# Kernel optimization log

Measured on AMD Instinct MI355X. Metric: run time of the kernel, lower is better.

Reference implementation:

```python
import jax, jax.numpy as jnp
import numpy as np

B, L, D = 2, 2048, 1024
H, K = 16, 16
HD = D // H


def setup_inputs() -> dict:
    key = jax.random.key(0)
    k1, k2, k3, k4, k5 = jax.random.split(key, 5)
    x = jax.random.normal(k1, (B, L, D), dtype=jnp.float32)
    # Linear weight (out_features, in_features), small init to keep logits sane
    w_in = jax.random.normal(k2, (3 * D, D), dtype=jnp.float32) * 0.02
    # TISA radial-basis kernel parameters, per (head, kernel)
    kernel_offsets = jax.random.normal(k3, (H, K), dtype=jnp.float32) * 20.0
    kernel_amplitudes = 0.1 + 0.01 * jax.random.normal(k4, (H, K), dtype=jnp.float32)
    kernel_sharpness = 0.1 + 0.01 * jax.random.normal(k5, (H, K), dtype=jnp.float32)
    return {"x": x, "w_in": w_in, "kernel_offsets": kernel_offsets,
            "kernel_amplitudes": kernel_amplitudes, "kernel_sharpness": kernel_sharpness}


def tisa_bias(offsets, amplitudes, sharpness, seq_len):
    # relative positions -(L-1) .. (L-1)  -> per-head RBF positional scores
    rel = jnp.arange(-(seq_len - 1), seq_len, dtype=jnp.float32)  # (2L-1,)
    # scores[h, m] = sum_k amp[h,k] * exp(-|sharp[h,k]| * (off[h,k] - rel[m])^2)
    diff = offsets[:, :, None] - rel[None, None, :]               # (H, K, 2L-1)
    scores = jnp.sum(amplitudes[:, :, None] * jnp.exp(-jnp.abs(sharpness)[:, :, None] * diff * diff), axis=1)  # (H, 2L-1)
    # Toeplitz expansion: bias[h, i, j] = scores[h, (i - j) + (L-1)]
    i = jnp.arange(seq_len)
    idx = i[:, None] - i[None, :] + (seq_len - 1)                 # (L, L)
    return scores[:, idx]                                         # (H, L, L)


def reference(x, w_in, kernel_offsets, kernel_amplitudes, kernel_sharpness):
    b, l, d = x.shape
    proj = jnp.einsum('bld,ed->ble', x, w_in)                     # (B, L, 3D)
    # split: memory = first 2D (k then v), query = last D
    k_, v_, q_ = proj[..., :d], proj[..., d:2 * d], proj[..., 2 * d:]

    def heads(t):
        return t.reshape(b, l, H, HD).transpose(0, 2, 1, 3)       # (B, H, L, HD)

    q, k, v = heads(q_), heads(k_), heads(v_)
    bias = tisa_bias(kernel_offsets, kernel_amplitudes, kernel_sharpness, l)  # (H, L, L)
    scale = 1.0 / np.sqrt(HD).astype(np.float32)
    logits = jnp.einsum('bhld,bhmd->bhlm', q, k) * scale + bias[None]
    attn = jax.nn.softmax(logits, axis=-1)
    out = jnp.einsum('bhlm,bhmd->bhld', attn, v)                  # (B, H, L, HD)
    return out.transpose(0, 2, 1, 3).reshape(b, l, d)             # (B, L, D)
```

## Files before the change

kernel.cpp:

```cpp
#include <hip/hip_runtime.h>
#include <hip/hip_bf16.h>
#include <stdint.h>
#include <stddef.h>


#define NB     2
#define NH     16
#define SL     2048
#define DH     64
#define DMODEL 1024
#define SCP    4096

typedef __attribute__((ext_vector_type(8)))  short bf16x8;
typedef __attribute__((ext_vector_type(4)))  short bf16x4;
typedef __attribute__((ext_vector_type(4)))  float f32x4;
typedef __attribute__((ext_vector_type(16))) float f32x16;

static __device__ __forceinline__ short f2bf(float x) {
  __hip_bfloat16 h = __float2bfloat16(x);
  return *reinterpret_cast<short*>(&h);
}
static __device__ __forceinline__ short f2bf_fast(float x) {
  union { float f; uint32_t u; } v; v.f = x;
  return (short)((v.u + 0x8000u) >> 16);
}
static __device__ __forceinline__ long long bf4_to_ll(bf16x4 v) {
  long long r; __builtin_memcpy(&r, &v, 8); return r;
}
static __device__ __forceinline__ bf16x4 ll_to_bf4(long long v) {
  bf16x4 r; __builtin_memcpy(&r, &v, 8); return r;
}
#define GLD(g, l) __builtin_amdgcn_global_load_lds( \
    (const __attribute__((address_space(1))) void*)(g), \
    (__attribute__((address_space(3))) void*)(l), 16, 0, 0)

__global__ __launch_bounds__(256) void prep_k(
    const float* __restrict__ x, const float* __restrict__ w,
    const float* __restrict__ koff, const float* __restrict__ kamp,
    const float* __restrict__ kshp,
    short* __restrict__ xbf, short* __restrict__ wbf,
    float* __restrict__ scores) {
  const int bx = blockIdx.x, tid = threadIdx.x;
  if (bx < 7168) {
    const float* src = (bx < 4096) ? x : w;
    short* dst       = (bx < 4096) ? xbf : wbf;
    const int i      = (bx < 4096 ? bx : bx - 4096) * 256 + tid;
    float4 a = *(const float4*)(src + (size_t)i * 4);
    bf16x4 o;
    o.x = f2bf(a.x); o.y = f2bf(a.y); o.z = f2bf(a.z); o.w = f2bf(a.w);
    *(bf16x4*)(dst + (size_t)i * 4) = o;
  } else {
    const int idx = bx - 7168;
    const int h = idx >> 4;
    const int r = (idx & 15) * 256 + tid;
    if (r >= 4095) return;
    float rel = (float)(r - (SL - 1));
    float acc = 0.f;
#pragma unroll
    for (int k = 0; k < 16; ++k) {
      float o = koff[h * 16 + k];
      float a = kamp[h * 16 + k];
      float s = fabsf(kshp[h * 16 + k]);
      float d = o - rel;
      acc += a * __expf(-s * d * d);
    }
    scores[h * SCP + r] = acc;
  }
}

__global__ __launch_bounds__(256) void qkv_gemm_k(
    const short* __restrict__ A, const short* __restrict__ Bw,
    __hip_bfloat16* __restrict__ kbuf, __hip_bfloat16* __restrict__ vbufT,
    __hip_bfloat16* __restrict__ qbuf) {
  __shared__ __align__(16) short SM[12288];
  short* As = SM;
  short* Bs = SM + 8192;
  const int tid  = threadIdx.x;
  const int lane = tid & 63;
  const int wv   = tid >> 6;
  const int l15  = lane & 15, quad = lane >> 4;
  const int wm = (wv & 1) * 64, wn = (wv >> 1) * 32;
  const int xt = blockIdx.x, yt = blockIdx.y;
  const int m0 = yt * 128, n0 = xt * 64;
  const int which = xt >> 4;
  const int hh    = xt & 15;

  f32x4 acc[4][2];
#pragma unroll
  for (int r = 0; r < 4; ++r)
#pragma unroll
    for (int c = 0; c < 2; ++c) acc[r][c] = (f32x4){0.f, 0.f, 0.f, 0.f};

  for (int kt = 0; kt < 16; ++kt) {
    const int k0 = kt * 64;
#pragma unroll
    for (int it = 0; it < 4; ++it) {
      const int e8  = it * 256 + tid;
      GLD(A + (size_t)(m0 + (e8 >> 3)) * DMODEL + k0 + (e8 & 7) * 8, &As[e8 * 8]);
    }
#pragma unroll
    for (int it = 0; it < 2; ++it) {
      const int e8  = it * 256 + tid;
      GLD(Bw + (size_t)(n0 + (e8 >> 3)) * DMODEL + k0 + (e8 & 7) * 8, &Bs[e8 * 8]);
    }
    __syncthreads();
#pragma unroll
    for (int ki = 0; ki < 64; ki += 32) {
      bf16x8 af[4], bfv[2];
#pragma unroll
      for (int r = 0; r < 4; ++r)
        af[r] = *(const bf16x8*)&As[(wm + r * 16 + l15) * 64 + ki + quad * 8];
#pragma unroll
      for (int c = 0; c < 2; ++c)
        bfv[c] = *(const bf16x8*)&Bs[(wn + c * 16 + l15) * 64 + ki + quad * 8];
#pragma unroll
      for (int r = 0; r < 4; ++r)
#pragma unroll
        for (int c = 0; c < 2; ++c)
          acc[r][c] = __builtin_amdgcn_mfma_f32_16x16x32_bf16(af[r], bfv[c], acc[r][c], 0, 0, 0);
    }
    __syncthreads();
  }

  const int bb  = m0 >> 11;
  const int llb = m0 & 2047;
  if (which != 1) {
    const float qs = (which == 2) ? 0.125f : 1.0f;
#pragma unroll
    for (int r = 0; r < 4; ++r)
#pragma unroll
      for (int c = 0; c < 2; ++c)
#pragma unroll
        for (int gg = 0; gg < 4; ++gg)
          SM[(wm + r * 16 + quad * 4 + gg) * 72 + wn + c * 16 + l15] =
              f2bf_fast(acc[r][c][gg] * qs);
    __syncthreads();
    __hip_bfloat16* dst = (which == 0) ? kbuf : qbuf;
#pragma unroll
    for (int i = 0; i < 4; ++i) {
      const int cidx = i * 256 + tid;
      const int m = cidx >> 3, ch = cidx & 7;
      bf16x8 val = *(const bf16x8*)&SM[m * 72 + ch * 8];
      *(bf16x8*)&dst[(((size_t)bb * NH + hh) * SL + llb + m) * DH + ch * 8] = val;
    }
  } else {
#pragma unroll
    for (int r = 0; r < 4; ++r)
#pragma unroll
      for (int c = 0; c < 2; ++c) {
        bf16x4 pk;
#pragma unroll
        for (int gg = 0; gg < 4; ++gg) pk[gg] = f2bf_fast(acc[r][c][gg]);
        *(bf16x4*)&SM[(wn + c * 16 + l15) * 136 + wm + r * 16 + quad * 4] = pk;
      }
    __syncthreads();
#pragma unroll
    for (int i = 0; i < 4; ++i) {
      const int cidx = i * 256 + tid;
      const int n = cidx >> 4, ch = cidx & 15;
      bf16x8 val = *(const bf16x8*)&SM[n * 136 + ch * 8];
      *(bf16x8*)&vbufT[(((size_t)bb * NH + hh) * DH + n) * SL + llb + ch * 8] = val;
    }
  }
}

__global__ __launch_bounds__(128, 2) void attn_k(
    const __hip_bfloat16* __restrict__ qbuf, const __hip_bfloat16* __restrict__ kbuf,
    const __hip_bfloat16* __restrict__ vbufT, const float* __restrict__ scores,
    float* __restrict__ out) {
  __shared__ __align__(16) short Ks[64 * 72];
  __shared__ __align__(16) short Vs[64 * 72];
  __shared__ __align__(16) float Bss[2112];
  const int bh   = blockIdx.x;
  const int b    = bh >> 4, h = bh & 15;
  const int tid  = threadIdx.x;
  const int lane = tid & 63;
  const int wv   = tid >> 6;
  const int n32  = lane & 31, hf = lane >> 5;
  const int i0b  = blockIdx.y * 64;
  const int i0   = i0b + wv * 32;
  const __hip_bfloat16* qb = qbuf + (size_t)bh * SL * DH;
  const short* kb = (const short*)(kbuf + (size_t)bh * SL * DH);
  const short* vb = (const short*)(vbufT + (size_t)bh * DH * SL);
  const float* sc = scores + h * SCP;

  {
    const float* bsrc = sc + i0b;
#pragma unroll
    for (int i = 0; i < 4; ++i)
      GLD(bsrc + (size_t)(i * 128 + tid) * 4, &Bss[(i * 128 + tid) * 4]);
    if (tid < 16) GLD(bsrc + (size_t)(512 + tid) * 4, &Bss[(512 + tid) * 4]);
  }

  bf16x8 qf[4];
#pragma unroll
  for (int kc = 0; kc < 4; ++kc)
    qf[kc] = *(const bf16x8*)&qb[(size_t)(i0 + n32) * DH + kc * 16 + hf * 8];

  f32x16 ot[2];
#pragma unroll
  for (int dt = 0; dt < 2; ++dt)
#pragma unroll
    for (int r = 0; r < 16; ++r) ot[dt][r] = 0.f;
  float lsum = 0.f;

  for (int j0 = 0; j0 < SL; j0 += 64) {
    {
      const short* ksrc = kb + (size_t)j0 * DH;
#pragma unroll
      for (int i = 0; i < 4; ++i) {
        int c = i * 128 + tid; int r = c / 9, s = c - r * 9;
        GLD(ksrc + (size_t)r * DH + s * 8, &Ks[c * 8]);
      }
      if (tid < 64) {
        int c = 512 + tid; int r = c / 9, s = c - r * 9;
        GLD(ksrc + (size_t)r * DH + s * 8, &Ks[c * 8]);
      }
    }
    {
#pragma unroll
      for (int i = 0; i < 4; ++i) {
        int c = i * 128 + tid; int r = c / 9, s = c - r * 9;
        GLD(vb + (size_t)r * SL + j0 + s * 8, &Vs[c * 8]);
      }
      if (tid < 64) {
        int c = 512 + tid; int r = c / 9, s = c - r * 9;
        GLD(vb + (size_t)r * SL + j0 + s * 8, &Vs[c * 8]);
      }
    }
    __syncthreads();

#pragma unroll
    for (int kt = 0; kt < 2; ++kt) {
      f32x16 st;
#pragma unroll
      for (int r = 0; r < 16; ++r) st[r] = 0.f;
#pragma unroll
      for (int kc = 0; kc < 4; ++kc) {
        bf16x8 kf = *(const bf16x8*)&Ks[(kt * 32 + n32) * 72 + kc * 16 + hf * 8];
        st = __builtin_amdgcn_mfma_f32_32x32x16_bf16(kf, qf[kc], st, 0, 0, 0);
      }
      bf16x4 pk[4];
      const int tb0 = wv * 32 + n32 - j0 - kt * 32 - 4 * hf + 2047;
#pragma unroll
      for (int g = 0; g < 4; ++g) {
        const int tb = tb0 - 8 * g;
#pragma unroll
        for (int i = 0; i < 4; ++i) {
          const float p = __expf(st[g * 4 + i] + Bss[tb - i]);
          lsum += p;
          pk[g][i] = f2bf_fast(p);
        }
      }
      long long s0 = hf ? bf4_to_ll(pk[0]) : bf4_to_ll(pk[1]);
      bf16x4 r0 = ll_to_bf4(__shfl_xor(s0, 32));
      bf16x8 pf0 = hf == 0 ? __builtin_shufflevector(pk[0], r0, 0, 1, 2, 3, 4, 5, 6, 7)
                           : __builtin_shufflevector(r0, pk[1], 0, 1, 2, 3, 4, 5, 6, 7);
      long long s1 = hf ? bf4_to_ll(pk[2]) : bf4_to_ll(pk[3]);
      bf16x4 r1 = ll_to_bf4(__shfl_xor(s1, 32));
      bf16x8 pf1 = hf == 0 ? __builtin_shufflevector(pk[2], r1, 0, 1, 2, 3, 4, 5, 6, 7)
                           : __builtin_shufflevector(r1, pk[3], 0, 1, 2, 3, 4, 5, 6, 7);
#pragma unroll
      for (int dt = 0; dt < 2; ++dt) {
        const short* vr = &Vs[(dt * 32 + n32) * 72 + kt * 32];
        bf16x8 vf0 = *(const bf16x8*)&vr[hf * 8];
        bf16x8 vf1 = *(const bf16x8*)&vr[16 + hf * 8];
        ot[dt] = __builtin_amdgcn_mfma_f32_32x32x16_bf16(vf0, pf0, ot[dt], 0, 0, 0);
        ot[dt] = __builtin_amdgcn_mfma_f32_32x32x16_bf16(vf1, pf1, ot[dt], 0, 0, 0);
      }
    }
    __syncthreads();
  }

  lsum += __shfl_xor(lsum, 32);
  const float inv = 1.f / lsum;
  float* orow = out + (((size_t)b * SL + i0 + n32) * NH + h) * DH;
#pragma unroll
  for (int dt = 0; dt < 2; ++dt)
#pragma unroll
    for (int g = 0; g < 4; ++g) {
      f32x4 v;
#pragma unroll
      for (int i = 0; i < 4; ++i) v[i] = ot[dt][g * 4 + i] * inv;
      *(f32x4*)&orow[dt * 32 + 8 * g + 4 * hf] = v;
    }
}

extern "C" void kernel_launch(void* const* d_in, const int* in_sizes, int n_in,
                              void* d_out, int out_size, void* d_ws, size_t ws_size,
                              hipStream_t stream) {
  const float* x    = (const float*)d_in[0];
  const float* w    = (const float*)d_in[1];
  const float* koff = (const float*)d_in[2];
  const float* kamp = (const float*)d_in[3];
  const float* kshp = (const float*)d_in[4];
  float* out = (float*)d_out;

  const size_t per = (size_t)NB * NH * SL * DH;
  const size_t nx  = (size_t)NB * SL * DMODEL;
  const size_t nw  = (size_t)3 * DMODEL * DMODEL;

  __hip_bfloat16* kbuf  = (__hip_bfloat16*)d_ws;
  __hip_bfloat16* vbufT = kbuf + per;
  __hip_bfloat16* qbuf  = vbufT + per;
  float* scores = (float*)(qbuf + per);
  short* xbf    = (short*)(scores + (size_t)NH * SCP);
  short* wbf    = xbf + nx;

  prep_k<<<7424, 256, 0, stream>>>(x, w, koff, kamp, kshp, xbf, wbf, scores);
  qkv_gemm_k<<<dim3(48, 32), 256, 0, stream>>>(xbf, wbf, kbuf, vbufT, qbuf);
  attn_k<<<dim3(NB * NH, SL / 64), 128, 0, stream>>>(qbuf, kbuf, vbufT, scores, out);
}
```

Before: 195.1 us.

## Double-buffer K/V tiles in attention and fold log2e into scores for exp2

The attention loop now double-buffers K, V and a small per-tile bias window in LDS, issuing the next tile's async global-to-LDS loads before computing the current tile. This hides load latency and keeps one barrier per iteration. Log2(e) is folded into the Q scale and the TISA scores so softmax can use the native exp2 instruction. s_setprio is raised around the MFMA sections. LDS use roughly doubles for K/V, which may affect occupancy, while the full bias slab is replaced by a 128-float window per tile.

```diff
diff --git a/kernel.cpp b/kernel.cpp
--- a/kernel.cpp
+++ b/kernel.cpp
@@ -10,6 +10,7 @@
 #define DH     64
 #define DMODEL 1024
 #define SCP    4096
+#define LOG2E  1.44269504088896340736f
 
 typedef __attribute__((ext_vector_type(8)))  short bf16x8;
 typedef __attribute__((ext_vector_type(4)))  short bf16x4;
@@ -29,6 +30,13 @@
 }
 static __device__ __forceinline__ bf16x4 ll_to_bf4(long long v) {
   bf16x4 r; __builtin_memcpy(&r, &v, 8); return r;
+}
+static __device__ __forceinline__ float fexp2(float x) {
+#if __has_builtin(__builtin_amdgcn_exp2f)
+  return __builtin_amdgcn_exp2f(x);
+#else
+  return __expf(x * 0.69314718056f);
+#endif
 }
 #define GLD(g, l) __builtin_amdgcn_global_load_lds( \
     (const __attribute__((address_space(1))) void*)(g), \
@@ -64,7 +72,7 @@
       float d = o - rel;
       acc += a * __expf(-s * d * d);
     }
-    scores[h * SCP + r] = acc;
+    scores[h * SCP + r] = acc * LOG2E;
   }
 }
 
@@ -125,7 +133,7 @@
   const int bb  = m0 >> 11;
   const int llb = m0 & 2047;
   if (which != 1) {
-    const float qs = (which == 2) ? 0.125f : 1.0f;
+    const float qs = (which == 2) ? 0.125f * LOG2E : 1.0f;
 #pragma unroll
     for (int r = 0; r < 4; ++r)
 #pragma unroll
@@ -168,9 +176,9 @@
     const __hip_bfloat16* __restrict__ qbuf, const __hip_bfloat16* __restrict__ kbuf,
     const __hip_bfloat16* __restrict__ vbufT, const float* __restrict__ scores,
     float* __restrict__ out) {
-  __shared__ __align__(16) short Ks[64 * 72];
-  __shared__ __align__(16) short Vs[64 * 72];
-  __shared__ __align__(16) float Bss[2112];
+  __shared__ __align__(16) short Ks[2][64 * 72];
+  __shared__ __align__(16) short Vs[2][64 * 72];
+  __shared__ __align__(16) float Bt[2][128];
   const int bh   = blockIdx.x;
   const int b    = bh >> 4, h = bh & 15;
   const int tid  = threadIdx.x;
@@ -184,14 +192,6 @@
   const short* vb = (const short*)(vbufT + (size_t)bh * DH * SL);
   const float* sc = scores + h * SCP;
 
-  {
-    const float* bsrc = sc + i0b;
-#pragma unroll
-    for (int i = 0; i < 4; ++i)
-      GLD(bsrc + (size_t)(i * 128 + tid) * 4, &Bss[(i * 128 + tid) * 4]);
-    if (tid < 16) GLD(bsrc + (size_t)(512 + tid) * 4, &Bss[(512 + tid) * 4]);
-  }
-
   bf16x8 qf[4];
 #pragma unroll
   for (int kc = 0; kc < 4; ++kc)
@@ -204,50 +204,53 @@
     for (int r = 0; r < 16; ++r) ot[dt][r] = 0.f;
   float lsum = 0.f;
 
-  for (int j0 = 0; j0 < SL; j0 += 64) {
-    {
-      const short* ksrc = kb + (size_t)j0 * DH;
-#pragma unroll
-      for (int i = 0; i < 4; ++i) {
-        int c = i * 128 + tid; int r = c / 9, s = c - r * 9;
-        GLD(ksrc + (size_t)r * DH + s * 8, &Ks[c * 8]);
-      }
-      if (tid < 64) {
-        int c = 512 + tid; int r = c / 9, s = c - r * 9;
-        GLD(ksrc + (size_t)r * DH + s * 8, &Ks[c * 8]);
-      }
-    }
-    {
-#pragma unroll
-      for (int i = 0; i < 4; ++i) {
-        int c = i * 128 + tid; int r = c / 9, s = c - r * 9;
-        GLD(vb + (size_t)r * SL + j0 + s * 8, &Vs[c * 8]);
-      }
-      if (tid < 64) {
-        int c = 512 + tid; int r = c / 9, s = c - r * 9;
-        GLD(vb + (size_t)r * SL + j0 + s * 8, &Vs[c * 8]);
-      }
-    }
-    __syncthreads();
-
+  auto stage = [&](int bsel, int j0) {
+    const short* ksrc = kb + (size_t)j0 * DH;
+#pragma unroll
+    for (int i = 0; i < 4; ++i) {
+      int c = i * 128 + tid; int r = c / 9, s = c - r * 9;
+      GLD(ksrc + (size_t)r * DH + s * 8, &Ks[bsel][c * 8]);
+    }
+    if (tid < 64) {
+      int c = 512 + tid; int r = c / 9, s = c - r * 9;
+      GLD(ksrc + (size_t)r * DH + s * 8, &Ks[bsel][c * 8]);
+    }
+#pragma unroll
+    for (int i = 0; i < 4; ++i) {
+      int c = i * 128 + tid; int r = c / 9, s = c - r * 9;
+      GLD(vb + (size_t)r * SL + j0 + s * 8, &Vs[bsel][c * 8]);
+    }
+    if (tid < 64) {
+      int c = 512 + tid; int r = c / 9, s = c - r * 9;
+      GLD(vb + (size_t)r * SL + j0 + s * 8, &Vs[bsel][c * 8]);
+    }
+    if (tid < 32) GLD(sc + (i0b - j0 + 1984) + tid * 4, &Bt[bsel][tid * 4]);
+  };
+
+  auto compute = [&](int bsel) {
+    const short* Kp = Ks[bsel];
+    const short* Vp = Vs[bsel];
+    const float* Bp = Bt[bsel];
 #pragma unroll
     for (int kt = 0; kt < 2; ++kt) {
       f32x16 st;
 #pragma unroll
       for (int r = 0; r < 16; ++r) st[r] = 0.f;
+      __builtin_amdgcn_s_setprio(1);
 #pragma unroll
       for (int kc = 0; kc < 4; ++kc) {
-        bf16x8 kf = *(const bf16x8*)&Ks[(kt * 32 + n32) * 72 + kc * 16 + hf * 8];
+        bf16x8 kf = *(const bf16x8*)&Kp[(kt * 32 + n32) * 72 + kc * 16 + hf * 8];
         st = __builtin_amdgcn_mfma_f32_32x32x16_bf16(kf, qf[kc], st, 0, 0, 0);
       }
+      __builtin_amdgcn_s_setprio(0);
       bf16x4 pk[4];
-      const int tb0 = wv * 32 + n32 - j0 - kt * 32 - 4 * hf + 2047;
+      const int tb0 = wv * 32 + n32 - kt * 32 - 4 * hf + 63;
 #pragma unroll
       for (int g = 0; g < 4; ++g) {
         const int tb = tb0 - 8 * g;
 #pragma unroll
         for (int i = 0; i < 4; ++i) {
-          const float p = __expf(st[g * 4 + i] + Bss[tb - i]);
+          const float p = fexp2(st[g * 4 + i] + Bp[tb - i]);
           lsum += p;
           pk[g][i] = f2bf_fast(p);
         }
@@ -260,17 +263,29 @@
       bf16x4 r1 = ll_to_bf4(__shfl_xor(s1, 32));
       bf16x8 pf1 = hf == 0 ? __builtin_shufflevector(pk[2], r1, 0, 1, 2, 3, 4, 5, 6, 7)
                            : __builtin_shufflevector(r1, pk[3], 0, 1, 2, 3, 4, 5, 6, 7);
+      __builtin_amdgcn_s_setprio(1);
 #pragma unroll
       for (int dt = 0; dt < 2; ++dt) {
-        const short* vr = &Vs[(dt * 32 + n32) * 72 + kt * 32];
+        const short* vr = &Vp[(dt * 32 + n32) * 72 + kt * 32];
         bf16x8 vf0 = *(const bf16x8*)&vr[hf * 8];
         bf16x8 vf1 = *(const bf16x8*)&vr[16 + hf * 8];
         ot[dt] = __builtin_amdgcn_mfma_f32_32x32x16_bf16(vf0, pf0, ot[dt], 0, 0, 0);
         ot[dt] = __builtin_amdgcn_mfma_f32_32x32x16_bf16(vf1, pf1, ot[dt], 0, 0, 0);
       }
-    }
-    __syncthreads();
+      __builtin_amdgcn_s_setprio(0);
+    }
+  };
+
+  stage(0, 0);
+  __syncthreads();
+  int cur = 0;
+  for (int j0 = 64; j0 < SL; j0 += 64) {
+    stage(cur ^ 1, j0);
+    compute(cur);
+    __syncthreads();
+    cur ^= 1;
   }
+  compute(cur);
 
   lsum += __shfl_xor(lsum, 32);
   const float inv = 1.f / lsum;
```

After: 187.1 us. 4.1% less time.
